# Kernel optimization log

Hardware: AMD Instinct MI355X
Metric: run time of the kernel (lower is better)

## Reference

```python
import jax, jax.numpy as jnp
import numpy as np

GRID_SIZE = 5
SPLINE_ORDER = 3
IN_SIZE = 257
HID = 40
NUM_LAYERS = 2
OUT_SIZE = 257
N_BASIS = GRID_SIZE + SPLINE_ORDER  # 8


def make_grid():
    # efficient-kan extended grid over [-1, 1]
    h = 2.0 / GRID_SIZE
    return (jnp.arange(-SPLINE_ORDER, GRID_SIZE + SPLINE_ORDER + 1, dtype=jnp.float32) * h - 1.0)


def b_splines(x, grid):
    # x: (..., in), grid: (G + 2k + 1,) -> (..., in, G + k) via Cox-de Boor
    x = x[..., None]
    b = ((x >= grid[:-1]) & (x < grid[1:])).astype(x.dtype)
    for k in range(1, SPLINE_ORDER + 1):
        b = ((x - grid[: -(k + 1)]) / (grid[k:-1] - grid[: -(k + 1)]) * b[..., :-1]
             + (grid[k + 1:] - x) / (grid[k + 1:] - grid[1:-k]) * b[..., 1:])
    return b


def gru_cell(x, h, Wih, Whh, bih, bhh):
    # torch.nn.GRUCell math, applied to every timestep at once.
    # x: (B,T,I), h: (B,T,H); Wih: (3H,I), Whh: (3H,H)
    gi = jnp.einsum('bti,gi->btg', x, Wih) + bih
    gh = jnp.einsum('bth,gh->btg', h, Whh) + bhh
    i_r, i_z, i_n = jnp.split(gi, 3, axis=-1)
    h_r, h_z, h_n = jnp.split(gh, 3, axis=-1)
    r = jax.nn.sigmoid(i_r + h_r)
    z = jax.nn.sigmoid(i_z + h_z)
    n = jnp.tanh(i_n + r * h_n)
    return (1.0 - z) * n + z * h


def kan_linear(x, base_weight, spline_weight, spline_scaler, grid):
    # efficient-kan KANLinear: SiLU base branch + B-spline branch
    base = jnp.einsum('bti,oi->bto', jax.nn.silu(x), base_weight)
    basis = b_splines(x, grid)  # (B,T,in,N_BASIS)
    w = spline_weight * spline_scaler[..., None]  # (out,in,N_BASIS)
    spl = jnp.einsum('btim,oim->bto', basis, w)
    return base + spl


def setup_inputs() -> dict:
    key = jax.random.key(0)
    ks = jax.random.split(key, 16)
    B, T = 64, 1000
    s = 0.1
    inp = {
        'x': jax.random.normal(ks[0], (B, T, IN_SIZE), dtype=jnp.float32),
        'Wih_f': jax.random.normal(ks[1], (NUM_LAYERS, 3 * HID, IN_SIZE), dtype=jnp.float32) * s,
        'Whh_f': jax.random.normal(ks[2], (NUM_LAYERS, 3 * HID, HID), dtype=jnp.float32) * s,
        'bih_f': jax.random.normal(ks[3], (NUM_LAYERS, 3 * HID), dtype=jnp.float32) * s,
        'bhh_f': jax.random.normal(ks[4], (NUM_LAYERS, 3 * HID), dtype=jnp.float32) * s,
        'Wih_b': jax.random.normal(ks[5], (NUM_LAYERS, 3 * HID, IN_SIZE), dtype=jnp.float32) * s,
        'Whh_b': jax.random.normal(ks[6], (NUM_LAYERS, 3 * HID, HID), dtype=jnp.float32) * s,
        'bih_b': jax.random.normal(ks[7], (NUM_LAYERS, 3 * HID), dtype=jnp.float32) * s,
        'bhh_b': jax.random.normal(ks[8], (NUM_LAYERS, 3 * HID), dtype=jnp.float32) * s,
        'base_weight': jax.random.normal(ks[9], (OUT_SIZE, 2 * HID), dtype=jnp.float32) * s,
        'spline_weight': jax.random.normal(ks[10], (OUT_SIZE, 2 * HID, N_BASIS), dtype=jnp.float32) * s,
        'spline_scaler': jnp.ones((OUT_SIZE, 2 * HID), dtype=jnp.float32),
        'slope': jnp.ones((OUT_SIZE,), dtype=jnp.float32),
        'lengths': jnp.full((B,), T, dtype=jnp.int32),
    }
    return inp


def reference(x, Wih_f, Whh_f, bih_f, bhh_f, Wih_b, Whh_b, bih_b, bhh_b,
              base_weight, spline_weight, spline_scaler, slope, lengths):
    B, T, _ = x.shape
    grid = make_grid()
    zeros_h = jnp.zeros((B, T, HID), dtype=x.dtype)
    # Forward-direction stack: layer 1 sees zero hidden (ht_f[0] is never
    # written in the source), layer 2 sees layer 1's same-timestep output.
    hf = zeros_h
    for l in range(NUM_LAYERS):
        hf = gru_cell(x, hf, Wih_f[l], Whh_f[l], bih_f[l], bhh_f[l])
    # Backward direction consumes x in reversed time order; out[:, i] pairs
    # hf(time i) with hb computed from x[:, T-1-i], i.e. hb in loop order.
    xb = x[:, ::-1, :]
    hb = zeros_h
    for l in range(NUM_LAYERS):
        hb = gru_cell(xb, hb, Wih_b[l], Whh_b[l], bih_b[l], bhh_b[l])
    feat = jnp.concatenate([hf, hb], axis=-1)  # (B,T,2H) == ht[-1]
    out = kan_linear(feat, base_weight, spline_weight, spline_scaler, grid)
    out = 1.2 * jax.nn.sigmoid(slope * out)
    return out
```

## Files before the change

kernel.cpp:

```cpp
#include <hip/hip_runtime.h>
#include <hip/hip_bf16.h>

#define B_    64
#define T_    1000
#define IN_   257
#define HID_  40
#define G3_   120
#define OUT_  257
#define M_    (B_*T_)
#define NGI_  480
#define KP_   736
#define KP1_  288
#define NP_   288

#define OFF_GI1 30720000ull
#define OFF_P   61440000ull
#define OFF_WK  (OFF_P + 94208000ull)
#define OFF_WB  (OFF_WK + 423936ull)
#define OFF_WHT (OFF_WB + 276480ull)
#define OFF_H0R (OFF_WHT + 32768ull)
#define OFF_H0C (OFF_H0R + 16384000ull)
#define OFF_GHC (OFF_H0C + 10240000ull)

typedef __attribute__((ext_vector_type(8))) short bfx8;
typedef __attribute__((ext_vector_type(4))) short bfx4;
typedef __attribute__((ext_vector_type(4))) float f32x4;

__device__ __forceinline__ float sigf(float x){ return 1.0f/(1.0f + __expf(-x)); }
__device__ __forceinline__ float tanhfast(float x){ return 1.0f - 2.0f/(__expf(2.0f*x)+1.0f); }

__device__ __forceinline__ short bfbits(float v){
    __hip_bfloat16 h = __float2bfloat16(v);
    return *(short*)&h;
}
__device__ __forceinline__ float b2f(short s){
    return __uint_as_float(((unsigned)(unsigned short)s) << 16);
}

__global__ __launch_bounds__(256) void kprep(const float* __restrict__ bw,
                                             const float* __restrict__ sw,
                                             const float* __restrict__ ss,
                                             __hip_bfloat16* __restrict__ wk){
    int idx = blockIdx.x*256 + threadIdx.x;
    if (idx >= NP_*(KP_/8)) return;
    int o = idx / (KP_/8), q = idx % (KP_/8);
    bfx8 pk;
#pragma unroll
    for (int e=0;e<8;e++){
        int k = q*8 + e;
        float v = 0.0f;
        if (o < OUT_ && k < 720){
            if (k < 80) v = bw[o*80 + k];
            else { int i = (k-80)>>3, m = (k-80)&7; v = sw[(o*80+i)*8 + m] * ss[o*80+i]; }
        }
        pk[e] = bfbits(v);
    }
    *(bfx8*)((void*)&wk[(size_t)o*KP_ + q*8]) = pk;
}

__global__ __launch_bounds__(256) void wprep(const float* __restrict__ Wf,
                                             const float* __restrict__ Wbk,
                                             const float* __restrict__ Whh_f,
                                             const float* __restrict__ Whh_b,
                                             const float* __restrict__ bhh_f,
                                             const float* __restrict__ bhh_b,
                                             __hip_bfloat16* __restrict__ wb,
                                             __hip_bfloat16* __restrict__ wht){
    int idx = blockIdx.x*256 + threadIdx.x;
    if (idx < NGI_*(KP1_/8)){
        int n = idx / (KP1_/8), q = idx % (KP1_/8);
        bfx8 pk;
#pragma unroll
        for (int e=0;e<8;e++){
            int k = q*8 + e;
            float v = 0.0f;
            if (k < IN_) v = (n < 240) ? Wf[(size_t)n*IN_ + k] : Wbk[(size_t)(n-240)*IN_ + k];
            pk[e] = bfbits(v);
        }
        *(bfx8*)((void*)&wb[(size_t)n*KP1_ + q*8]) = pk;
        return;
    }
    int i2 = idx - NGI_*(KP1_/8);
    if (i2 >= 2*128*8) return;
    int d = i2 >> 10;
    int rest = i2 & 1023;
    int gate = rest >> 3, q = rest & 7;
    const float* Whh = d ? Whh_b : Whh_f;
    const float* bhh = d ? bhh_b : bhh_f;
    bfx8 pk;
#pragma unroll
    for (int e=0;e<8;e++){
        int k = q*8 + e;
        float v = 0.0f;
        if (gate < G3_){
            if (k < 40) v = Whh[G3_*HID_ + gate*HID_ + k];
            else if (k == 40) v = bhh[G3_ + gate];
        }
        pk[e] = bfbits(v);
    }
    *(bfx8*)((void*)&wht[(size_t)(d*128 + gate)*64 + q*8]) = pk;
}

__global__ __launch_bounds__(256) void k1_gemm(const float* __restrict__ X,
                                               const __hip_bfloat16* __restrict__ Wb16,
                                               const float* __restrict__ bf,
                                               const float* __restrict__ bb,
                                               __hip_bfloat16* __restrict__ gi0,
                                               __hip_bfloat16* __restrict__ gi1){
    __shared__ __hip_bfloat16 Asm[9*64*40];
    int tid = threadIdx.x, wave = tid>>6, lane = tid&63;
    int wr = wave>>1, wc = wave&1;
    int rl = lane&15, kq = lane>>4;
    int m0 = blockIdx.x*64;

    {
        int r = tid>>2, slot = tid&3;
#pragma unroll
        for (int ks=0;ks<9;ks++){
            int kg = ks*32 + slot*8;
            const float* xp = &X[(size_t)(m0+r)*IN_ + kg];
            bfx8 pk;
            if (kg + 7 < IN_){
                f32x4 x0 = *(const f32x4*)xp;
                f32x4 x1 = *(const f32x4*)(xp+4);
#pragma unroll
                for (int e=0;e<4;e++){ pk[e] = bfbits(x0[e]); pk[4+e] = bfbits(x1[e]); }
            } else {
#pragma unroll
                for (int e=0;e<8;e++){ int k = kg + e; pk[e] = (k < IN_) ? bfbits(xp[e]) : (short)0; }
            }
            *(bfx8*)((void*)&Asm[(ks*64 + r)*40 + slot*8]) = pk;
        }
    }
    __syncthreads();

    f32x4 acc[2][15];
#pragma unroll
    for (int f=0;f<2;f++)
#pragma unroll
        for (int j=0;j<15;j++) acc[f][j] = (f32x4){0.f,0.f,0.f,0.f};

    for (int ks=0; ks<9; ++ks){
        bfx8 a0 = *(bfx8*)((void*)&Asm[(ks*64 + wr*32 + rl)*40 + kq*8]);
        bfx8 a1 = *(bfx8*)((void*)&Asm[(ks*64 + wr*32 + 16 + rl)*40 + kq*8]);
        const __hip_bfloat16* bp = &Wb16[(size_t)(wc*240 + rl)*KP1_ + ks*32 + kq*8];
#pragma unroll
        for (int j=0;j<15;j++){
            bfx8 b = *(const bfx8*)&bp[(size_t)j*16*KP1_];
            acc[0][j] = __builtin_amdgcn_mfma_f32_16x16x32_bf16(a0, b, acc[0][j], 0,0,0);
            acc[1][j] = __builtin_amdgcn_mfma_f32_16x16x32_bf16(a1, b, acc[1][j], 0,0,0);
        }
    }

#pragma unroll
    for (int j=0;j<15;j++){
        int n = wc*240 + j*16 + rl;
        float bias = (n < 240) ? bf[n] : bb[n-240];
        int d  = (n >= 240) ? 1 : 0;
        int nn = n - 240*d;
#pragma unroll
        for (int f=0;f<2;f++){
            int mb = m0 + wr*32 + f*16 + kq*4;
            bfx4 v;
#pragma unroll
            for (int r=0;r<4;r++) v[r] = bfbits(acc[f][j][r] + bias);
            if (nn < 120){
                *(bfx4*)((void*)&gi0[(size_t)(d*120 + nn)*M_ + mb]) = v;
            } else {
                *(bfx4*)((void*)&gi1[(size_t)(d*120 + nn - 120)*M_ + mb]) = v;
            }
        }
    }
}

__global__ __launch_bounds__(256) void k2a(const __hip_bfloat16* __restrict__ gi0,
                                           const float* __restrict__ bhh_f,
                                           const float* __restrict__ bhh_b,
                                           __hip_bfloat16* __restrict__ h0R,
                                           __hip_bfloat16* __restrict__ h0C){
    int blk = blockIdx.x;
    int dir = (blk >= 250) ? 1 : 0;
    int m = (blk - dir*250)*256 + threadIdx.x;
    int b = m / T_, t = m - b*T_;
    int src = dir ? (b*T_ + (T_-1-t)) : m;
    const float* bhh0v = dir ? bhh_b : bhh_f;

    const __hip_bfloat16* g0 = gi0 + (size_t)(dir*120)*M_ + src;
    __hip_bfloat16* hc = h0C + (size_t)(dir*40)*M_ + m;
    float h0[HID_];
#pragma unroll
    for (int j=0;j<HID_;j++){
        float ir = b2f(*(const short*)&g0[(size_t)j*M_]);
        float iz = b2f(*(const short*)&g0[(size_t)(40+j)*M_]);
        float in = b2f(*(const short*)&g0[(size_t)(80+j)*M_]);
        float r = sigf(ir + bhh0v[j]);
        float z = sigf(iz + bhh0v[40+j]);
        float n = tanhfast(in + r*bhh0v[80+j]);
        h0[j] = (1.0f - z)*n;
        hc[(size_t)j*M_] = __float2bfloat16(h0[j]);
    }
    __hip_bfloat16* hr = h0R + (size_t)(dir*M_ + m)*64;
#pragma unroll
    for (int q=0;q<8;q++){
        bfx8 v;
#pragma unroll
        for (int e=0;e<8;e++){
            int idx = q*8 + e;
            float f = (idx < HID_) ? h0[idx] : (idx == HID_ ? 1.0f : 0.0f);
            v[e] = bfbits(f);
        }
        *(bfx8*)((void*)&hr[q*8]) = v;
    }
}

__global__ __launch_bounds__(512) void k2b(const __hip_bfloat16* __restrict__ h0R,
                                           const __hip_bfloat16* __restrict__ WhT,
                                           __hip_bfloat16* __restrict__ ghC){
    __shared__ __hip_bfloat16 Ah[256*64];
    __shared__ __hip_bfloat16 Bh[128*64];
    int tid = threadIdx.x, wave = tid>>6, lane = tid&63;
    int wr = wave>>1, wc = wave&1;
    int rl = lane&15, kq = lane>>4;
    int blk = blockIdx.x;
    int dir = (blk >= 250) ? 1 : 0;
    int m0 = (blk - dir*250)*256;

#pragma unroll
    for (int p=0;p<4;p++){
        int c = tid + p*512;
        int row = c>>3, q = c&7;
        bfx8 v = *(const bfx8*)&h0R[(size_t)(dir*M_ + m0 + row)*64 + q*8];
        *(bfx8*)((void*)&Ah[row*64 + ((q ^ (row&7))<<3)]) = v;
    }
#pragma unroll
    for (int p=0;p<2;p++){
        int c = tid + p*512;
        int row = c>>3, q = c&7;
        bfx8 v = *(const bfx8*)&WhT[(size_t)(dir*128 + row)*64 + q*8];
        *(bfx8*)((void*)&Bh[row*64 + ((q ^ (row&7))<<3)]) = v;
    }
    __syncthreads();

    f32x4 acc[4][4];
#pragma unroll
    for (int f=0;f<4;f++)
#pragma unroll
        for (int j=0;j<4;j++) acc[f][j] = (f32x4){0.f,0.f,0.f,0.f};

#pragma unroll
    for (int ks=0;ks<2;ks++){
        bfx8 a[4], bb[4];
#pragma unroll
        for (int f=0;f<4;f++){
            int row = wr*64 + f*16 + rl;
            a[f] = *(bfx8*)((void*)&Ah[row*64 + (((ks*4+kq) ^ (row&7))<<3)]);
        }
#pragma unroll
        for (int j=0;j<4;j++){
            int row = wc*64 + j*16 + rl;
            bb[j] = *(bfx8*)((void*)&Bh[row*64 + (((ks*4+kq) ^ (row&7))<<3)]);
        }
#pragma unroll
        for (int f=0;f<4;f++)
#pragma unroll
            for (int j=0;j<4;j++)
                acc[f][j] = __builtin_amdgcn_mfma_f32_16x16x32_bf16(a[f], bb[j], acc[f][j], 0,0,0);
    }
#pragma unroll
    for (int j=0;j<4;j++){
        int n = wc*64 + j*16 + rl;
        if (n < G3_){
#pragma unroll
            for (int f=0;f<4;f++){
                int mb = m0 + wr*64 + f*16 + kq*4;
                bfx4 v;
#pragma unroll
                for (int r=0;r<4;r++) v[r] = bfbits(acc[f][j][r]);
                *(bfx4*)((void*)&ghC[(size_t)(dir*G3_ + n)*M_ + mb]) = v;
            }
        }
    }
}

__global__ __launch_bounds__(256, 4) void k2c(const __hip_bfloat16* __restrict__ gi1,
                                              const __hip_bfloat16* __restrict__ ghC,
                                              const __hip_bfloat16* __restrict__ h0C,
                                              __hip_bfloat16* __restrict__ P){
    int tid = threadIdx.x;
    int bb = blockIdx.x;
    int mblk = bb % 250;
    int rest = bb / 250;
    int dir = rest / 5, grp = rest % 5;
    int m = mblk*256 + tid;
    int b = m / T_, t = m - b*T_;
    int src = dir ? (b*T_ + (T_-1-t)) : m;

    const __hip_bfloat16* g1 = gi1 + (size_t)(dir*120)*M_ + src;
    const __hip_bfloat16* gh = ghC + (size_t)(dir*120)*M_ + m;
    const __hip_bfloat16* hc = h0C + (size_t)(dir*40)*M_ + m;

    bfx8 sil;
#pragma unroll
    for (int jj=0;jj<8;jj++){
        int j = grp*8 + jj;
        float ir = b2f(*(const short*)&g1[(size_t)j*M_]);
        float iz = b2f(*(const short*)&g1[(size_t)(40+j)*M_]);
        float in = b2f(*(const short*)&g1[(size_t)(80+j)*M_]);
        float gr = b2f(*(const short*)&gh[(size_t)j*M_]);
        float gz = b2f(*(const short*)&gh[(size_t)(40+j)*M_]);
        float gn = b2f(*(const short*)&gh[(size_t)(80+j)*M_]);
        float r = sigf(ir + gr);
        float z = sigf(iz + gz);
        float n = tanhfast(in + r*gn);
        float h1 = (1.0f - z)*n + z*b2f(*(const short*)&hc[(size_t)j*M_]);
        sil[jj] = bfbits(h1 * sigf(h1));

        float tt = (h1 + 1.0f) * 2.5f;
        float fs = floorf(tt);
        fs = fminf(fmaxf(fs, 0.0f), 4.0f);
        int sp = (int)fs;
        float u  = tt - fs;
        float um = 1.0f - u;
        float u2 = u*u, u3 = u2*u;
        float N0 = um*um*um * (1.0f/6.0f);
        float N1 = (3.0f*u3 - 6.0f*u2 + 4.0f) * (1.0f/6.0f);
        float N2 = (-3.0f*u3 + 3.0f*u2 + 3.0f*u + 1.0f) * (1.0f/6.0f);
        float N3 = u3 * (1.0f/6.0f);
        bfx8 pk;
#pragma unroll
        for (int i=0;i<8;i++){
            int d = i - sp;
            float v = (d==0)?N0 : (d==1)?N1 : (d==2)?N2 : (d==3)?N3 : 0.0f;
            pk[i] = bfbits(v);
        }
        *(bfx8*)((void*)&P[((size_t)(10 + dir*40 + j)*M_ + m)*8]) = pk;
    }
    *(bfx8*)((void*)&P[((size_t)(dir*5 + grp)*M_ + m)*8]) = sil;
    if (dir==0 && grp==0){
        bfx8 z8 = {0,0,0,0,0,0,0,0};
        *(bfx8*)((void*)&P[((size_t)90*M_ + m)*8]) = z8;
        *(bfx8*)((void*)&P[((size_t)91*M_ + m)*8]) = z8;
    }
}

__global__ __launch_bounds__(512) void k3_gemm(const __hip_bfloat16* __restrict__ P,
                                               const __hip_bfloat16* __restrict__ Wk,
                                               const float* __restrict__ slope,
                                               float* __restrict__ outp){
    __shared__ __hip_bfloat16 Asm[2][256*40];
    __shared__ __hip_bfloat16 Bsm[2][NP_*40];
    int tid = threadIdx.x, wave = tid>>6, lane = tid&63;
    int wr = wave>>1, wc = wave&1;
    int rl = lane&15, kq = lane>>4;
    int m0 = blockIdx.x*256;

    int qA = tid>>8, rA = tid&255;
    int rB = tid>>2, qB = tid&3;

    f32x4 acc[4][9];
#pragma unroll
    for (int f=0;f<4;f++)
#pragma unroll
        for (int j=0;j<9;j++) acc[f][j] = (f32x4){0.f,0.f,0.f,0.f};

    bfx8 ra[2], rb[3];

#define K3_LOAD(tt) { \
    int k8 = (tt)*4, k0 = (tt)*32; \
    ra[0] = *(const bfx8*)&P[((size_t)(k8+qA)*M_ + m0 + rA)*8]; \
    ra[1] = *(const bfx8*)&P[((size_t)(k8+qA+2)*M_ + m0 + rA)*8]; \
    rb[0] = *(const bfx8*)&Wk[(size_t)rB*KP_ + k0 + qB*8]; \
    rb[1] = *(const bfx8*)&Wk[(size_t)(rB+128)*KP_ + k0 + qB*8]; \
    if (tid < 128) rb[2] = *(const bfx8*)&Wk[(size_t)(rB+256)*KP_ + k0 + qB*8]; }

#define K3_WRITE(bufi) { \
    *(bfx8*)((void*)&Asm[bufi][rA*40 + qA*8]) = ra[0]; \
    *(bfx8*)((void*)&Asm[bufi][rA*40 + (qA+2)*8]) = ra[1]; \
    *(bfx8*)((void*)&Bsm[bufi][rB*40 + qB*8]) = rb[0]; \
    *(bfx8*)((void*)&Bsm[bufi][(rB+128)*40 + qB*8]) = rb[1]; \
    if (tid < 128) *(bfx8*)((void*)&Bsm[bufi][(rB+256)*40 + qB*8]) = rb[2]; }

    K3_LOAD(0); K3_WRITE(0); __syncthreads();
    for (int t=0; t<23; ++t){
        int c = t&1;
        if (t < 22) K3_LOAD(t+1);
        bfx8 a[4];
#pragma unroll
        for (int f=0;f<4;f++)
            a[f] = *(bfx8*)((void*)&Asm[c][(wr*64 + f*16 + rl)*40 + kq*8]);
#pragma unroll
        for (int j=0;j<9;j++){
            bfx8 b = *(bfx8*)((void*)&Bsm[c][(wc*144 + j*16 + rl)*40 + kq*8]);
#pragma unroll
            for (int f=0;f<4;f++)
                acc[f][j] = __builtin_amdgcn_mfma_f32_16x16x32_bf16(a[f], b, acc[f][j], 0,0,0);
        }
        if (t < 22) K3_WRITE(c^1);
        __syncthreads();
    }
#pragma unroll
    for (int j=0;j<9;j++){
        int n = wc*144 + j*16 + rl;
        if (n < OUT_){
            float sl = slope[n];
#pragma unroll
            for (int f=0;f<4;f++){
                int mb = m0 + wr*64 + f*16 + kq*4;
#pragma unroll
                for (int r=0;r<4;r++)
                    outp[(size_t)(mb+r)*OUT_ + n] = 1.2f * sigf(sl*acc[f][j][r]);
            }
        }
    }
}

extern "C" void kernel_launch(void* const* d_in, const int* in_sizes, int n_in,
                              void* d_out, int out_size, void* d_ws, size_t ws_size,
                              hipStream_t stream) {
    const float* x      = (const float*)d_in[0];
    const float* Wih_f  = (const float*)d_in[1];
    const float* Whh_f  = (const float*)d_in[2];
    const float* bih_f  = (const float*)d_in[3];
    const float* bhh_f  = (const float*)d_in[4];
    const float* Wih_b  = (const float*)d_in[5];
    const float* Whh_b  = (const float*)d_in[6];
    const float* bih_b  = (const float*)d_in[7];
    const float* bhh_b  = (const float*)d_in[8];
    const float* base_w = (const float*)d_in[9];
    const float* spl_w  = (const float*)d_in[10];
    const float* spl_s  = (const float*)d_in[11];
    const float* slope  = (const float*)d_in[12];

    char* ws = (char*)d_ws;
    __hip_bfloat16* gi0 = (__hip_bfloat16*)ws;
    __hip_bfloat16* gi1 = (__hip_bfloat16*)(ws + OFF_GI1);
    __hip_bfloat16* P   = (__hip_bfloat16*)(ws + OFF_P);
    __hip_bfloat16* Wk  = (__hip_bfloat16*)(ws + OFF_WK);
    __hip_bfloat16* Wb  = (__hip_bfloat16*)(ws + OFF_WB);
    __hip_bfloat16* WhT = (__hip_bfloat16*)(ws + OFF_WHT);
    __hip_bfloat16* h0R = (__hip_bfloat16*)(ws + OFF_H0R);
    __hip_bfloat16* h0C = (__hip_bfloat16*)(ws + OFF_H0C);
    __hip_bfloat16* ghC = (__hip_bfloat16*)(ws + OFF_GHC);
    float* outp = (float*)d_out;

    hipLaunchKernelGGL(kprep, dim3((NP_*(KP_/8) + 255)/256), dim3(256), 0, stream,
                       base_w, spl_w, spl_s, Wk);
    hipLaunchKernelGGL(wprep, dim3((NGI_*(KP1_/8) + 2048 + 255)/256), dim3(256), 0, stream,
                       Wih_f, Wih_b, Whh_f, Whh_b, bhh_f, bhh_b, Wb, WhT);
    hipLaunchKernelGGL(k1_gemm, dim3(1000), dim3(256), 0, stream,
                       x, Wb, bih_f, bih_b, gi0, gi1);
    hipLaunchKernelGGL(k2a, dim3(500), dim3(256), 0, stream,
                       gi0, bhh_f, bhh_b, h0R, h0C);
    hipLaunchKernelGGL(k2b, dim3(500), dim3(512), 0, stream,
                       h0R, WhT, ghC);
    hipLaunchKernelGGL(k2c, dim3(2500), dim3(256), 0, stream,
                       gi1, ghC, h0C, P);
    hipLaunchKernelGGL(k3_gemm, dim3(250), dim3(512), 0, stream,
                       P, Wk, slope, outp);
}
```

Measured before the change: 364.8 us.

## Double-buffer input-projection GEMM with LDS-staged weights and larger row tiles

The first GEMM (x times the GRU input weights) now uses 512-thread blocks covering 128 rows each. Per 32-wide K step, the A tile and the full 480-column B weight slice are staged into LDS. Global loads for the next K step are prefetched into registers and overlapped with the MFMA work on the current buffer, replacing the old scheme that loaded all of A up front and read B straight from global memory. This cuts redundant global weight reads and hides load latency, at the cost of more LDS and a barrier every step. The LDS row stride of 40 may cause bank conflicts.

```diff
diff --git a/kernel.cpp b/kernel.cpp
--- a/kernel.cpp
+++ b/kernel.cpp
@@ -101,55 +101,73 @@
     *(bfx8*)((void*)&wht[(size_t)(d*128 + gate)*64 + q*8]) = pk;
 }
 
-__global__ __launch_bounds__(256) void k1_gemm(const float* __restrict__ X,
+__global__ __launch_bounds__(512) void k1_gemm(const float* __restrict__ X,
                                                const __hip_bfloat16* __restrict__ Wb16,
                                                const float* __restrict__ bf,
                                                const float* __restrict__ bb,
                                                __hip_bfloat16* __restrict__ gi0,
                                                __hip_bfloat16* __restrict__ gi1){
-    __shared__ __hip_bfloat16 Asm[9*64*40];
+    __shared__ __hip_bfloat16 Asm[2][128*40];
+    __shared__ __hip_bfloat16 Bsm[2][480*40];
     int tid = threadIdx.x, wave = tid>>6, lane = tid&63;
     int wr = wave>>1, wc = wave&1;
     int rl = lane&15, kq = lane>>4;
-    int m0 = blockIdx.x*64;
-
-    {
-        int r = tid>>2, slot = tid&3;
-#pragma unroll
-        for (int ks=0;ks<9;ks++){
-            int kg = ks*32 + slot*8;
-            const float* xp = &X[(size_t)(m0+r)*IN_ + kg];
-            bfx8 pk;
-            if (kg + 7 < IN_){
-                f32x4 x0 = *(const f32x4*)xp;
-                f32x4 x1 = *(const f32x4*)(xp+4);
-#pragma unroll
-                for (int e=0;e<4;e++){ pk[e] = bfbits(x0[e]); pk[4+e] = bfbits(x1[e]); }
-            } else {
-#pragma unroll
-                for (int e=0;e<8;e++){ int k = kg + e; pk[e] = (k < IN_) ? bfbits(xp[e]) : (short)0; }
-            }
-            *(bfx8*)((void*)&Asm[(ks*64 + r)*40 + slot*8]) = pk;
-        }
-    }
-    __syncthreads();
-
+    int m0 = blockIdx.x*128;
+
+    int rA = tid>>2, qA = tid&3;
     f32x4 acc[2][15];
 #pragma unroll
     for (int f=0;f<2;f++)
 #pragma unroll
         for (int j=0;j<15;j++) acc[f][j] = (f32x4){0.f,0.f,0.f,0.f};
 
-    for (int ks=0; ks<9; ++ks){
-        bfx8 a0 = *(bfx8*)((void*)&Asm[(ks*64 + wr*32 + rl)*40 + kq*8]);
-        bfx8 a1 = *(bfx8*)((void*)&Asm[(ks*64 + wr*32 + 16 + rl)*40 + kq*8]);
-        const __hip_bfloat16* bp = &Wb16[(size_t)(wc*240 + rl)*KP1_ + ks*32 + kq*8];
+    bfx8 ra, rb[4];
+
+#define K1_LOAD(tt) { \
+    int k0 = (tt)*32; \
+    { int kg = k0 + qA*8; \
+      const float* xp = &X[(size_t)(m0+rA)*IN_ + kg]; \
+      if (kg + 7 < IN_){ \
+          f32x4 x0 = *(const f32x4*)xp; \
+          f32x4 x1 = *(const f32x4*)(xp+4); \
+          _Pragma("unroll") \
+          for (int e=0;e<4;e++){ ra[e] = bfbits(x0[e]); ra[4+e] = bfbits(x1[e]); } \
+      } else { \
+          _Pragma("unroll") \
+          for (int e=0;e<8;e++){ int k = kg + e; ra[e] = (k < IN_) ? bfbits(xp[e]) : (short)0; } \
+      } } \
+    _Pragma("unroll") \
+    for (int p=0;p<4;p++){ \
+        int ci = tid + p*512; \
+        if (ci < 1920){ \
+            int r = ci>>2, q = ci&3; \
+            rb[p] = *(const bfx8*)&Wb16[(size_t)r*KP1_ + k0 + q*8]; \
+        } } }
+
+#define K1_WRITE(bufi) { \
+    *(bfx8*)((void*)&Asm[bufi][rA*40 + qA*8]) = ra; \
+    _Pragma("unroll") \
+    for (int p=0;p<4;p++){ \
+        int ci = tid + p*512; \
+        if (ci < 1920){ \
+            int r = ci>>2, q = ci&3; \
+            *(bfx8*)((void*)&Bsm[bufi][r*40 + q*8]) = rb[p]; \
+        } } }
+
+    K1_LOAD(0); K1_WRITE(0); __syncthreads();
+    for (int t=0; t<9; ++t){
+        int c = t&1;
+        if (t < 8) K1_LOAD(t+1);
+        bfx8 a0 = *(bfx8*)((void*)&Asm[c][(wr*32 + rl)*40 + kq*8]);
+        bfx8 a1 = *(bfx8*)((void*)&Asm[c][(wr*32 + 16 + rl)*40 + kq*8]);
 #pragma unroll
         for (int j=0;j<15;j++){
-            bfx8 b = *(const bfx8*)&bp[(size_t)j*16*KP1_];
+            bfx8 b = *(bfx8*)((void*)&Bsm[c][(wc*240 + j*16 + rl)*40 + kq*8]);
             acc[0][j] = __builtin_amdgcn_mfma_f32_16x16x32_bf16(a0, b, acc[0][j], 0,0,0);
             acc[1][j] = __builtin_amdgcn_mfma_f32_16x16x32_bf16(a1, b, acc[1][j], 0,0,0);
         }
+        if (t < 8) K1_WRITE(c^1);
+        __syncthreads();
     }
 
 #pragma unroll
@@ -227,15 +245,15 @@
 
 #pragma unroll
     for (int p=0;p<4;p++){
-        int c = tid + p*512;
-        int row = c>>3, q = c&7;
+        int cc = tid + p*512;
+        int row = cc>>3, q = cc&7;
         bfx8 v = *(const bfx8*)&h0R[(size_t)(dir*M_ + m0 + row)*64 + q*8];
         *(bfx8*)((void*)&Ah[row*64 + ((q ^ (row&7))<<3)]) = v;
     }
 #pragma unroll
     for (int p=0;p<2;p++){
-        int c = tid + p*512;
-        int row = c>>3, q = c&7;
+        int cc = tid + p*512;
+        int row = cc>>3, q = cc&7;
         bfx8 v = *(const bfx8*)&WhT[(size_t)(dir*128 + row)*64 + q*8];
         *(bfx8*)((void*)&Bh[row*64 + ((q ^ (row&7))<<3)]) = v;
     }
@@ -447,7 +465,7 @@
                        base_w, spl_w, spl_s, Wk);
     hipLaunchKernelGGL(wprep, dim3((NGI_*(KP1_/8) + 2048 + 255)/256), dim3(256), 0, stream,
                        Wih_f, Wih_b, Whh_f, Whh_b, bhh_f, bhh_b, Wb, WhT);
-    hipLaunchKernelGGL(k1_gemm, dim3(1000), dim3(256), 0, stream,
+    hipLaunchKernelGGL(k1_gemm, dim3(500), dim3(512), 0, stream,
                        x, Wb, bih_f, bih_b, gi0, gi1);
     hipLaunchKernelGGL(k2a, dim3(500), dim3(256), 0, stream,
                        gi0, bhh_f, bhh_b, h0R, h0C);
```

Result: faster. 312.8 us (-14.3%).
